# Kernel optimization log

Hardware: AMD Instinct MI355X
Metric: run time of the kernel (lower is better)

Reference implementation:

```python
import jax, jax.numpy as jnp
import numpy as np

N_NODES = 100000
N_EDGES = 3200000
D_NODE = 128
D_EDGE = 16


def setup_inputs() -> dict:
    key = jax.random.key(0)
    k1, k2, k3, k4, k5, k6, k7 = jax.random.split(key, 7)
    nodes = jax.random.normal(k1, (N_NODES, D_NODE), dtype=jnp.float32)
    edges = jax.random.normal(k2, (N_EDGES, D_EDGE), dtype=jnp.float32)
    senders = jax.random.randint(k3, (N_EDGES,), 0, N_NODES, dtype=jnp.int32)
    receivers = jax.random.randint(k4, (N_EDGES,), 0, N_NODES, dtype=jnp.int32)
    w_node = jax.random.normal(k5, (), dtype=jnp.float32)
    w_edge = jax.random.normal(k6, (), dtype=jnp.float32)
    b_node = jax.random.normal(k7, (), dtype=jnp.float32)
    return {
        "nodes": nodes,
        "edges": edges,
        "senders": senders,
        "receivers": receivers,
        "w_node": w_node,
        "w_edge": w_edge,
        "b_node": b_node,
    }


def reference(nodes, edges, senders, receivers, w_node, w_edge, b_node):
    # gather sender node scalar feature (column 0): [E]
    sender_vals = nodes[senders, 0]
    edge_vals = edges[:, 0]  # [E]
    # per-edge message: scalar mult-add
    messages = w_edge * edge_vals + w_node * sender_vals  # [E]
    # scatter-add into receivers: [N]
    agg = jax.ops.segment_sum(messages, receivers, num_segments=nodes.shape[0])
    return w_node * nodes[:, 0] + agg + b_node
```

## Files before the change

kernel.cpp:

```cpp
#include <hip/hip_runtime.h>

#define N_NODES 100000
#define N_EDGES 3200000
#define D_NODE 128
#define D_EDGE 16

#define NR 7
#define SPAN 16384
#define CAP 560000
#define NSLICE 64

#define K1_THREADS 256
#define K1_EDGES 512
#define NW (K1_THREADS / 64)
#define K1_ROUNDS (K1_EDGES / K1_THREADS)

#define WS_X     0
#define WS_CNT   100000
#define WS_OVF   100008
#define WS_BKT   200008
#define WS_PART  (WS_BKT + NR * CAP * 2)
#define WS_TOTAL (WS_PART + NSLICE * N_NODES)

typedef int   iv2 __attribute__((ext_vector_type(2)));
typedef int   iv4 __attribute__((ext_vector_type(4)));
typedef float fv4 __attribute__((ext_vector_type(4)));

__global__ void v4_init(const float* __restrict__ nodes,
                        float* __restrict__ x,
                        float* __restrict__ ovf,
                        int*   __restrict__ cnt) {
    int i = blockIdx.x * blockDim.x + threadIdx.x;
    if (i < 8) cnt[i] = 0;
    if (i < N_NODES) {
        x[i]   = nodes[(size_t)i * D_NODE];
        ovf[i] = 0.f;
    }
}

__global__ __launch_bounds__(K1_THREADS) void v4_bucketize(
        const float* __restrict__ x,
        const float* __restrict__ edges,
        const int*   __restrict__ senders,
        const int*   __restrict__ receivers,
        const float* __restrict__ w_node,
        const float* __restrict__ w_edge,
        int*   __restrict__ cnt,
        float* __restrict__ ovf,
        int*   __restrict__ bkt) {
    __shared__ iv2 s_pair[NR][K1_EDGES];
    __shared__ int s_wcnt[NW][NR];
    __shared__ int s_wbase[NW][NR];
    __shared__ int s_fill[NR];
    __shared__ int s_gbase[NR];

    const float wn = w_node[0];
    const float we = w_edge[0];
    const int tile = blockIdx.x * K1_EDGES;
    const int lane = threadIdx.x & 63;
    const int wv   = threadIdx.x >> 6;
    const unsigned long long lt = (1ull << lane) - 1ull;

    if (threadIdx.x < NR) s_fill[threadIdx.x] = 0;

    int rr[K1_ROUNDS]; float mm[K1_ROUNDS];
#pragma unroll
    for (int j = 0; j < K1_ROUNDS; ++j) {
        int e    = tile + j * K1_THREADS + (int)threadIdx.x;
        rr[j]    = __builtin_nontemporal_load(receivers + e);
        int s    = __builtin_nontemporal_load(senders + e);
        float ev = __builtin_nontemporal_load(edges + (size_t)e * D_EDGE);
        mm[j] = we * ev + wn * x[s];
    }
    __syncthreads();

#pragma unroll
    for (int j = 0; j < K1_ROUNDS; ++j) {
        const int b = rr[j] >> 14;
        int rank = 0, wcount = 0;
#pragma unroll
        for (int k = 0; k < NR; ++k) {
            unsigned long long mk = __ballot(b == k);
            if (k == b)    rank   = __popcll(mk & lt);
            if (lane == k) wcount = __popcll(mk);
        }
        if (lane < NR) s_wcnt[wv][lane] = wcount;
        __syncthreads();
        if (threadIdx.x < NR) {
            int bb = threadIdx.x;
            int base = s_fill[bb];
#pragma unroll
            for (int w = 0; w < NW; ++w) { s_wbase[w][bb] = base; base += s_wcnt[w][bb]; }
            s_fill[bb] = base;
        }
        __syncthreads();
        iv2 v; v.x = rr[j] & (SPAN - 1); v.y = __float_as_int(mm[j]);
        s_pair[b][s_wbase[wv][b] + rank] = v;
        __syncthreads();
    }

    if (threadIdx.x < NR)
        s_gbase[threadIdx.x] = atomicAdd(&cnt[threadIdx.x], s_fill[threadIdx.x]);
    __syncthreads();

#pragma unroll
    for (int b = 0; b < NR; ++b) {
        const int n  = s_fill[b];
        const int gb = s_gbase[b];
        if (gb + n <= CAP) {
            for (int i = threadIdx.x; i < n; i += K1_THREADS)
                *(iv2*)(bkt + ((size_t)b * CAP + gb + i) * 2) = s_pair[b][i];
        } else {
            for (int i = threadIdx.x; i < n; i += K1_THREADS) {
                iv2 v = s_pair[b][i];
                int gi = gb + i;
                if (gi < CAP) *(iv2*)(bkt + ((size_t)b * CAP + gi) * 2) = v;
                else atomicAdd(&ovf[b * SPAN + v.x], __int_as_float(v.y));
            }
        }
    }
}

__global__ __launch_bounds__(1024) void v4_accum(
        const int* __restrict__ bkt,
        const int* __restrict__ cnt,
        float* __restrict__ partials) {
    extern __shared__ float acc[];
    const int r  = blockIdx.y;
    const int lo = r * SPAN;
    int span = N_NODES - lo; if (span > SPAN) span = SPAN;

    const int n     = cnt[r];
    const int chunk = (n + NSLICE - 1) / NSLICE;
    int start = blockIdx.x * chunk;
    int end   = start + chunk; if (end > n) end = n;

    for (int i = threadIdx.x * 4; i < SPAN; i += 4096) {
        fv4 z = {0.f, 0.f, 0.f, 0.f};
        *(fv4*)(acc + i) = z;
    }
    __syncthreads();

    const int* base = bkt + (size_t)r * CAP * 2;
    for (int i = start + (int)threadIdx.x; i < end; i += 1024) {
        iv2 v = *(const iv2*)(base + (size_t)i * 2);
        atomicAdd(&acc[v.x], __int_as_float(v.y));
    }
    __syncthreads();

    float* dst = partials + (size_t)blockIdx.x * N_NODES + lo;
    for (int i = threadIdx.x * 4; i < span; i += 4096)
        *(fv4*)(dst + i) = *(const fv4*)(acc + i);
}

__global__ void v4_out(const float* __restrict__ x,
                       const float* __restrict__ partials,
                       const float* __restrict__ ovf,
                       const float* __restrict__ w_node,
                       const float* __restrict__ b_node,
                       float* __restrict__ out) {
    int i = blockIdx.x * blockDim.x + threadIdx.x;
    if (i >= N_NODES) return;
    float s = w_node[0] * x[i] + b_node[0] + ovf[i];
#pragma unroll 8
    for (int c = 0; c < NSLICE; ++c) s += partials[(size_t)c * N_NODES + i];
    out[i] = s;
}

__global__ void tmp_init_out(const float* __restrict__ nodes,
                             const float* __restrict__ w_node,
                             const float* __restrict__ b_node,
                             float* __restrict__ out) {
    int i = blockIdx.x * blockDim.x + threadIdx.x;
    if (i < N_NODES) out[i] = w_node[0] * nodes[(size_t)i * D_NODE] + b_node[0];
}

__global__ void tmp_edge_scatter_direct(const float* __restrict__ nodes,
                                        const float* __restrict__ edges,
                                        const int*   __restrict__ senders,
                                        const int*   __restrict__ receivers,
                                        const float* __restrict__ w_node,
                                        const float* __restrict__ w_edge,
                                        float* __restrict__ out) {
    const float wn = w_node[0];
    const float we = w_edge[0];
    int base = (blockIdx.x * blockDim.x + threadIdx.x) * 4;
    if (base + 3 < N_EDGES) {
        iv4 s = *(const iv4*)(senders + base);
        iv4 r = *(const iv4*)(receivers + base);
        atomicAdd(&out[r.x], we * edges[(size_t)(base + 0) * D_EDGE] + wn * nodes[(size_t)s.x * D_NODE]);
        atomicAdd(&out[r.y], we * edges[(size_t)(base + 1) * D_EDGE] + wn * nodes[(size_t)s.y * D_NODE]);
        atomicAdd(&out[r.z], we * edges[(size_t)(base + 2) * D_EDGE] + wn * nodes[(size_t)s.z * D_NODE]);
        atomicAdd(&out[r.w], we * edges[(size_t)(base + 3) * D_EDGE] + wn * nodes[(size_t)s.w * D_NODE]);
    } else {
        for (int e = base; e < N_EDGES; ++e) {
            atomicAdd(&out[receivers[e]],
                      we * edges[(size_t)e * D_EDGE] + wn * nodes[(size_t)senders[e] * D_NODE]);
        }
    }
}

extern "C" void kernel_launch(void* const* d_in, const int* in_sizes, int n_in,
                              void* d_out, int out_size, void* d_ws, size_t ws_size,
                              hipStream_t stream) {
    const float* nodes     = (const float*)d_in[0];
    const float* edges     = (const float*)d_in[1];
    const int*   senders   = (const int*)d_in[2];
    const int*   receivers = (const int*)d_in[3];
    const float* w_node    = (const float*)d_in[4];
    const float* w_edge    = (const float*)d_in[5];
    const float* b_node    = (const float*)d_in[6];
    float* out = (float*)d_out;
    float* ws  = (float*)d_ws;

    if (ws_size >= (size_t)WS_TOTAL * sizeof(float)) {
        float* x    = ws + WS_X;
        int*   cnt  = (int*)(ws + WS_CNT);
        float* ovf  = ws + WS_OVF;
        int*   bkt  = (int*)(ws + WS_BKT);
        float* part = ws + WS_PART;

        int threads = 256;
        v4_init<<<(N_NODES + threads - 1) / threads, threads, 0, stream>>>(
            nodes, x, ovf, cnt);

        v4_bucketize<<<N_EDGES / K1_EDGES, K1_THREADS, 0, stream>>>(
            x, edges, senders, receivers, w_node, w_edge, cnt, ovf, bkt);

        dim3 grid2(NSLICE, NR);
        v4_accum<<<grid2, 1024, SPAN * sizeof(float), stream>>>(bkt, cnt, part);

        v4_out<<<(N_NODES + threads - 1) / threads, threads, 0, stream>>>(
            x, part, ovf, w_node, b_node, out);
    } else {
        int threads = 256;
        tmp_init_out<<<(N_NODES + threads - 1) / threads, threads, 0, stream>>>(
            nodes, w_node, b_node, out);
        int n_thr = N_EDGES / 4;
        tmp_edge_scatter_direct<<<(n_thr + threads - 1) / threads, threads, 0, stream>>>(
            nodes, edges, senders, receivers, w_node, w_edge, out);
    }
}
```

Baseline: 389.6 us.

## Write bucketed edges directly to global memory, skipping the shared staging buffer

The bucketize kernel no longer stages (receiver, message) pairs in shared memory per bucket with three block barriers per round. It now computes per-wave, per-round bucket ranks with ballots, does one prefix scan plus a global atomic reservation per bucket, and writes each pair straight to its global bucket slot. Each block also takes 1024 edges instead of 512. This removes most barriers and the shared-memory round trip, but the global writes become scattered across seven bucket streams and are less coalesced.

```diff
diff --git a/kernel.cpp b/kernel.cpp
--- a/kernel.cpp
+++ b/kernel.cpp
@@ -11,7 +11,7 @@
 #define NSLICE 64
 
 #define K1_THREADS 256
-#define K1_EDGES 512
+#define K1_EDGES 1024
 #define NW (K1_THREADS / 64)
 #define K1_ROUNDS (K1_EDGES / K1_THREADS)
 
@@ -26,7 +26,7 @@
 typedef int   iv4 __attribute__((ext_vector_type(4)));
 typedef float fv4 __attribute__((ext_vector_type(4)));
 
-__global__ void v4_init(const float* __restrict__ nodes,
+__global__ void v5_init(const float* __restrict__ nodes,
                         float* __restrict__ x,
                         float* __restrict__ ovf,
                         int*   __restrict__ cnt) {
@@ -38,7 +38,7 @@
     }
 }
 
-__global__ __launch_bounds__(K1_THREADS) void v4_bucketize(
+__global__ __launch_bounds__(K1_THREADS) void v5_bucketize(
         const float* __restrict__ x,
         const float* __restrict__ edges,
         const int*   __restrict__ senders,
@@ -48,80 +48,68 @@
         int*   __restrict__ cnt,
         float* __restrict__ ovf,
         int*   __restrict__ bkt) {
-    __shared__ iv2 s_pair[NR][K1_EDGES];
-    __shared__ int s_wcnt[NW][NR];
-    __shared__ int s_wbase[NW][NR];
-    __shared__ int s_fill[NR];
+    __shared__ int s_cnt[NW][K1_ROUNDS][NR];
+    __shared__ int s_off[NW][K1_ROUNDS][NR];
     __shared__ int s_gbase[NR];
 
     const float wn = w_node[0];
     const float we = w_edge[0];
     const int tile = blockIdx.x * K1_EDGES;
-    const int lane = threadIdx.x & 63;
-    const int wv   = threadIdx.x >> 6;
+    const int tid  = (int)threadIdx.x;
+    const int lane = tid & 63;
+    const int wv   = tid >> 6;
     const unsigned long long lt = (1ull << lane) - 1ull;
 
-    if (threadIdx.x < NR) s_fill[threadIdx.x] = 0;
-
     int rr[K1_ROUNDS]; float mm[K1_ROUNDS];
 #pragma unroll
     for (int j = 0; j < K1_ROUNDS; ++j) {
-        int e    = tile + j * K1_THREADS + (int)threadIdx.x;
+        int e    = tile + j * K1_THREADS + tid;
         rr[j]    = __builtin_nontemporal_load(receivers + e);
         int s    = __builtin_nontemporal_load(senders + e);
         float ev = __builtin_nontemporal_load(edges + (size_t)e * D_EDGE);
         mm[j] = we * ev + wn * x[s];
     }
-    __syncthreads();
-
+
+    int rk[K1_ROUNDS]; int wc[K1_ROUNDS];
 #pragma unroll
     for (int j = 0; j < K1_ROUNDS; ++j) {
         const int b = rr[j] >> 14;
-        int rank = 0, wcount = 0;
+        int rank = 0, cnt_k = 0;
 #pragma unroll
         for (int k = 0; k < NR; ++k) {
             unsigned long long mk = __ballot(b == k);
-            if (k == b)    rank   = __popcll(mk & lt);
-            if (lane == k) wcount = __popcll(mk);
+            if (k == b)    rank  = __popcll(mk & lt);
+            if (lane == k) cnt_k = __popcll(mk);
         }
-        if (lane < NR) s_wcnt[wv][lane] = wcount;
-        __syncthreads();
-        if (threadIdx.x < NR) {
-            int bb = threadIdx.x;
-            int base = s_fill[bb];
-#pragma unroll
-            for (int w = 0; w < NW; ++w) { s_wbase[w][bb] = base; base += s_wcnt[w][bb]; }
-            s_fill[bb] = base;
-        }
-        __syncthreads();
+        rk[j] = rank; wc[j] = cnt_k;
+    }
+    if (lane < NR) {
+#pragma unroll
+        for (int j = 0; j < K1_ROUNDS; ++j) s_cnt[wv][j][lane] = wc[j];
+    }
+    __syncthreads();
+
+    if (tid < NR) {
+        int base = 0;
+#pragma unroll
+        for (int j = 0; j < K1_ROUNDS; ++j)
+#pragma unroll
+            for (int w = 0; w < NW; ++w) { s_off[w][j][tid] = base; base += s_cnt[w][j][tid]; }
+        s_gbase[tid] = atomicAdd(&cnt[tid], base);
+    }
+    __syncthreads();
+
+#pragma unroll
+    for (int j = 0; j < K1_ROUNDS; ++j) {
+        const int b = rr[j] >> 14;
+        int pos = s_gbase[b] + s_off[wv][j][b] + rk[j];
         iv2 v; v.x = rr[j] & (SPAN - 1); v.y = __float_as_int(mm[j]);
-        s_pair[b][s_wbase[wv][b] + rank] = v;
-        __syncthreads();
-    }
-
-    if (threadIdx.x < NR)
-        s_gbase[threadIdx.x] = atomicAdd(&cnt[threadIdx.x], s_fill[threadIdx.x]);
-    __syncthreads();
-
-#pragma unroll
-    for (int b = 0; b < NR; ++b) {
-        const int n  = s_fill[b];
-        const int gb = s_gbase[b];
-        if (gb + n <= CAP) {
-            for (int i = threadIdx.x; i < n; i += K1_THREADS)
-                *(iv2*)(bkt + ((size_t)b * CAP + gb + i) * 2) = s_pair[b][i];
-        } else {
-            for (int i = threadIdx.x; i < n; i += K1_THREADS) {
-                iv2 v = s_pair[b][i];
-                int gi = gb + i;
-                if (gi < CAP) *(iv2*)(bkt + ((size_t)b * CAP + gi) * 2) = v;
-                else atomicAdd(&ovf[b * SPAN + v.x], __int_as_float(v.y));
-            }
-        }
-    }
-}
-
-__global__ __launch_bounds__(1024) void v4_accum(
+        if (pos < CAP) *(iv2*)(bkt + ((size_t)b * CAP + pos) * 2) = v;
+        else atomicAdd(&ovf[b * SPAN + v.x], __int_as_float(v.y));
+    }
+}
+
+__global__ __launch_bounds__(1024) void v5_accum(
         const int* __restrict__ bkt,
         const int* __restrict__ cnt,
         float* __restrict__ partials) {
@@ -153,7 +141,7 @@
         *(fv4*)(dst + i) = *(const fv4*)(acc + i);
 }
 
-__global__ void v4_out(const float* __restrict__ x,
+__global__ void v5_out(const float* __restrict__ x,
                        const float* __restrict__ partials,
                        const float* __restrict__ ovf,
                        const float* __restrict__ w_node,
@@ -221,16 +209,16 @@
         float* part = ws + WS_PART;
 
         int threads = 256;
-        v4_init<<<(N_NODES + threads - 1) / threads, threads, 0, stream>>>(
+        v5_init<<<(N_NODES + threads - 1) / threads, threads, 0, stream>>>(
             nodes, x, ovf, cnt);
 
-        v4_bucketize<<<N_EDGES / K1_EDGES, K1_THREADS, 0, stream>>>(
+        v5_bucketize<<<N_EDGES / K1_EDGES, K1_THREADS, 0, stream>>>(
             x, edges, senders, receivers, w_node, w_edge, cnt, ovf, bkt);
 
         dim3 grid2(NSLICE, NR);
-        v4_accum<<<grid2, 1024, SPAN * sizeof(float), stream>>>(bkt, cnt, part);
-
-        v4_out<<<(N_NODES + threads - 1) / threads, threads, 0, stream>>>(
+        v5_accum<<<grid2, 1024, SPAN * sizeof(float), stream>>>(bkt, cnt, part);
+
+        v5_out<<<(N_NODES + threads - 1) / threads, threads, 0, stream>>>(
             x, part, ovf, w_node, b_node, out);
     } else {
         int threads = 256;
```

Result: faster. 358.3 us (-8.0%).
